# Optimization experiments

Hardware: AMD Instinct MI355X
Metric: run time of the kernel (lower is better)

## Reference

```python
import jax, jax.numpy as jnp
import numpy as np

B = 1_048_576
DIM = 64
NCI_TOTAL = 150_000
FMA_TOTAL = 100_000


def setup_inputs() -> dict:
    key = jax.random.key(0)
    k1, k2, k3, k4, k5, k6, k7 = jax.random.split(key, 7)
    return {
        "pos_n": jax.random.randint(k1, (B,), 0, NCI_TOTAL, dtype=jnp.int64) if jax.config.jax_enable_x64 else jax.random.randint(k1, (B,), 0, NCI_TOTAL, dtype=jnp.int32),
        "pos_m": jax.random.randint(k2, (B,), 0, NCI_TOTAL, dtype=jnp.int32),
        "pos_f": jax.random.randint(k3, (B,), 0, FMA_TOTAL, dtype=jnp.int32),
        "nci_emb": jax.random.normal(k4, (NCI_TOTAL, DIM), dtype=jnp.float32),
        "fma_emb": jax.random.normal(k5, (FMA_TOTAL, DIM), dtype=jnp.float32),
        "n2f_mat": jax.random.normal(k6, (DIM, DIM), dtype=jnp.float32) / np.sqrt(DIM),
        "m2f_mat": jax.random.normal(k7, (DIM, DIM), dtype=jnp.float32) / np.sqrt(DIM),
    }


def reference(pos_n, pos_m, pos_f, nci_emb, fma_emb, n2f_mat, m2f_mat):
    # Embedding gathers. In the original, transfer-matrix lookup ids are all
    # zeros, so the single [dim, dim] matrix is shared across the batch.
    n_e = nci_emb[pos_n]  # [B, D]
    m_e = nci_emb[pos_m]  # [B, D]  (note: pos_m also indexes nci table, per source)
    f_e = fma_emb[pos_f]  # [B, D]

    # TransR-style projection: h = M @ e per sample (shared M).
    h_n = jnp.einsum("ij,bj->bi", n2f_mat, n_e)  # [B, D]
    h_m = jnp.einsum("ij,bj->bi", m2f_mat, m_e)  # [B, D]

    # Squared-diff, sum over dim (the reduce_mean over a size-1 axis is a no-op),
    # then sum over batch.
    n2f_loss = jnp.sum(jnp.square(h_n - f_e))
    m2f_loss = jnp.sum(jnp.square(h_m - f_e))
    return n2f_loss + m2f_loss
```

## Files before the change

kernel.cpp:

```cpp
#include <hip/hip_runtime.h>
#include <hip/hip_fp16.h>


typedef _Float16 half8 __attribute__((ext_vector_type(8)));
typedef __fp16  fp16x2 __attribute__((ext_vector_type(2)));
typedef float floatx16 __attribute__((ext_vector_type(16)));

#define NBLOCKS 1024
#define SPB 128
#define NCI_ELEMS 9600000
#define FMA_ELEMS 6400000

__device__ inline half8 cvt8(float4 a, float4 b) {
    union { half8 h; fp16x2 h2[4]; } u;
    u.h2[0] = __builtin_amdgcn_cvt_pkrtz(a.x, a.y);
    u.h2[1] = __builtin_amdgcn_cvt_pkrtz(a.z, a.w);
    u.h2[2] = __builtin_amdgcn_cvt_pkrtz(b.x, b.y);
    u.h2[3] = __builtin_amdgcn_cvt_pkrtz(b.z, b.w);
    return u.h;
}

__device__ inline uint2 pack4(float4 v) {
    union { fp16x2 h2[2]; uint2 u; } p;
    p.h2[0] = __builtin_amdgcn_cvt_pkrtz(v.x, v.y);
    p.h2[1] = __builtin_amdgcn_cvt_pkrtz(v.z, v.w);
    return p.u;
}

__device__ inline uint2 pack8_fp8(float4 a, float4 b) {
    int lo = 0, hi = 0;
    lo = __builtin_amdgcn_cvt_pk_fp8_f32(a.x, a.y, lo, false);
    lo = __builtin_amdgcn_cvt_pk_fp8_f32(a.z, a.w, lo, true);
    hi = __builtin_amdgcn_cvt_pk_fp8_f32(b.x, b.y, hi, false);
    hi = __builtin_amdgcn_cvt_pk_fp8_f32(b.z, b.w, hi, true);
    uint2 r; r.x = (unsigned)lo; r.y = (unsigned)hi; return r;
}

__device__ inline long pack8_fp8_l(const float* p) {
    uint2 b = pack8_fp8(*(const float4*)p, *(const float4*)(p + 4));
    return (long)(((unsigned long)b.y << 32) | b.x);
}

__global__ __launch_bounds__(256) void convert_kernel(
    const float4* __restrict__ nci, const float4* __restrict__ fma,
    uint2* __restrict__ nci8, uint2* __restrict__ fma8)
{
    const int stride = gridDim.x * blockDim.x;
    const int tid = blockIdx.x * blockDim.x + threadIdx.x;
    for (int i = tid; i < NCI_ELEMS / 8; i += stride)
        nci8[i] = pack8_fp8(nci[2 * i], nci[2 * i + 1]);
    for (int i = tid; i < FMA_ELEMS / 8; i += stride)
        fma8[i] = pack8_fp8(fma[2 * i], fma[2 * i + 1]);
}

__global__ __launch_bounds__(256, 4) void ontomap_kernel_q(
    const int* __restrict__ pos_n, const int* __restrict__ pos_m,
    const int* __restrict__ pos_f,
    const unsigned char* __restrict__ nci8, const unsigned char* __restrict__ fma8,
    const float* __restrict__ n2f, const float* __restrict__ m2f,
    float* __restrict__ out, int iters)
{
    const int lane = threadIdx.x & 63;
    const int wave = threadIdx.x >> 6;
    const int l31  = lane & 31;
    const int hi   = lane >> 5;
    const int hoff = hi * 32;

    long Bn[2][4], Bm[2][4];
#pragma unroll
    for (int nt = 0; nt < 2; ++nt) {
#pragma unroll
        for (int t = 0; t < 4; ++t) {
            Bn[nt][t] = pack8_fp8_l(n2f + (nt * 32 + l31) * 64 + hoff + t * 8);
            Bm[nt][t] = pack8_fp8_l(m2f + (nt * 32 + l31) * 64 + hoff + t * 8);
        }
    }

    long If0[4], If1[4];
#pragma unroll
    for (int t = 0; t < 4; ++t) {
        const unsigned j = (unsigned)(l31 - t * 8);
        const long pat = (j < 8) ? (long)(0xB8ULL << (8 * j)) : 0L;
        If0[t] = hi ? 0L : pat;
        If1[t] = hi ? pat : 0L;
    }

    float loss = 0.0f;

    int in_, im_, if_;
    {
        int s = blockIdx.x * SPB + wave * 32 + l31;
        in_ = pos_n[s]; im_ = pos_m[s]; if_ = pos_f[s];
    }

#pragma unroll 1
    for (int it = 0; it < iters; ++it) {
        const int in0 = in_, im0 = im_, if0 = if_;
        if (it + 1 < iters) {
            int s = ((it + 1) * NBLOCKS + blockIdx.x) * SPB + wave * 32 + l31;
            in_ = pos_n[s]; im_ = pos_m[s]; if_ = pos_f[s];
        }

        const unsigned char* pn = nci8 + (long)in0 * 64 + hoff;
        const unsigned char* pf = fma8 + (long)if0 * 64 + hoff;
        const unsigned char* pm = nci8 + (long)im0 * 64 + hoff;

        ulonglong2 n01 = *(const ulonglong2*)pn;
        ulonglong2 n23 = *(const ulonglong2*)(pn + 16);
        ulonglong2 f01 = *(const ulonglong2*)pf;
        ulonglong2 f23 = *(const ulonglong2*)(pf + 16);
        ulonglong2 m01 = *(const ulonglong2*)pm;
        ulonglong2 m23 = *(const ulonglong2*)(pm + 16);

        const long An[4] = {(long)n01.x, (long)n01.y, (long)n23.x, (long)n23.y};
        const long Ff[4] = {(long)f01.x, (long)f01.y, (long)f23.x, (long)f23.y};
        const long Am[4] = {(long)m01.x, (long)m01.y, (long)m23.x, (long)m23.y};

        {
            floatx16 a{};
#pragma unroll
            for (int t = 0; t < 4; ++t)
                a = __builtin_amdgcn_mfma_f32_32x32x16_fp8_fp8(An[t], Bn[0][t], a, 0, 0, 0);
#pragma unroll
            for (int t = 0; t < 4; ++t)
                a = __builtin_amdgcn_mfma_f32_32x32x16_fp8_fp8(Ff[t], If0[t], a, 0, 0, 0);
#pragma unroll
            for (int r = 0; r < 16; ++r) loss = fmaf(a[r], a[r], loss);
        }
        {
            floatx16 a{};
#pragma unroll
            for (int t = 0; t < 4; ++t)
                a = __builtin_amdgcn_mfma_f32_32x32x16_fp8_fp8(An[t], Bn[1][t], a, 0, 0, 0);
#pragma unroll
            for (int t = 0; t < 4; ++t)
                a = __builtin_amdgcn_mfma_f32_32x32x16_fp8_fp8(Ff[t], If1[t], a, 0, 0, 0);
#pragma unroll
            for (int r = 0; r < 16; ++r) loss = fmaf(a[r], a[r], loss);
        }
        {
            floatx16 a{};
#pragma unroll
            for (int t = 0; t < 4; ++t)
                a = __builtin_amdgcn_mfma_f32_32x32x16_fp8_fp8(Am[t], Bm[0][t], a, 0, 0, 0);
#pragma unroll
            for (int t = 0; t < 4; ++t)
                a = __builtin_amdgcn_mfma_f32_32x32x16_fp8_fp8(Ff[t], If0[t], a, 0, 0, 0);
#pragma unroll
            for (int r = 0; r < 16; ++r) loss = fmaf(a[r], a[r], loss);
        }
        {
            floatx16 a{};
#pragma unroll
            for (int t = 0; t < 4; ++t)
                a = __builtin_amdgcn_mfma_f32_32x32x16_fp8_fp8(Am[t], Bm[1][t], a, 0, 0, 0);
#pragma unroll
            for (int t = 0; t < 4; ++t)
                a = __builtin_amdgcn_mfma_f32_32x32x16_fp8_fp8(Ff[t], If1[t], a, 0, 0, 0);
#pragma unroll
            for (int r = 0; r < 16; ++r) loss = fmaf(a[r], a[r], loss);
        }
    }

#pragma unroll
    for (int o = 32; o > 0; o >>= 1) loss += __shfl_xor(loss, o, 64);
    if (lane == 0) atomicAdd(out, loss);
}

#define ROW_BYTES 144
__global__ __launch_bounds__(256, 2) void ontomap_kernel_f32(
    const int* __restrict__ pos_n, const int* __restrict__ pos_m,
    const int* __restrict__ pos_f,
    const float* __restrict__ nci, const float* __restrict__ fma_emb,
    const float* __restrict__ n2f, const float* __restrict__ m2f,
    float* __restrict__ out, int iters)
{
    __shared__ char lds[4 * 2 * 32 * ROW_BYTES];

    const int lane = threadIdx.x & 63;
    const int wave = threadIdx.x >> 6;
    const int l31  = lane & 31;
    const int hi   = lane >> 5;
    const int kbase = hi * 8;
    const int srow   = lane >> 4;
    const int schunk = lane & 15;

    char* const nbase = lds + wave * (2 * 32 * ROW_BYTES);
    char* const mbase = nbase + 32 * ROW_BYTES;

    half8 Bn[2][4], Bm[2][4];
#pragma unroll
    for (int nt = 0; nt < 2; ++nt) {
#pragma unroll
        for (int t = 0; t < 4; ++t) {
            const float* p = n2f + (nt * 32 + l31) * 64 + t * 16 + kbase;
            Bn[nt][t] = cvt8(*(const float4*)p, *(const float4*)(p + 4));
            const float* q = m2f + (nt * 32 + l31) * 64 + t * 16 + kbase;
            Bm[nt][t] = cvt8(*(const float4*)q, *(const float4*)(q + 4));
        }
    }

    float loss = 0.0f;
    int in_, im_, if_;
    {
        int s = blockIdx.x * SPB + wave * 32 + l31;
        in_ = pos_n[s]; im_ = pos_m[s]; if_ = pos_f[s];
    }

#pragma unroll 1
    for (int it = 0; it < iters; ++it) {
        const int in0 = in_, im0 = im_, if0 = if_;
        if (it + 1 < iters) {
            int s = ((it + 1) * NBLOCKS + blockIdx.x) * SPB + wave * 32 + l31;
            in_ = pos_n[s]; im_ = pos_m[s]; if_ = pos_f[s];
        }

#pragma unroll
        for (int i = 0; i < 8; ++i) {
            const int rl = i * 4 + srow;
            const int rn = __shfl(in0, rl, 64);
            float4 v = ((const float4*)(nci + (long)rn * 64))[schunk];
            *(uint2*)(nbase + rl * ROW_BYTES + schunk * 8) = pack4(v);
            const int rm = __shfl(im0, rl, 64);
            float4 w = ((const float4*)(nci + (long)rm * 64))[schunk];
            *(uint2*)(mbase + rl * ROW_BYTES + schunk * 8) = pack4(w);
        }
        asm volatile("" ::: "memory");

        floatx16 aN0{}, aN1{}, aM0{}, aM1{};
#pragma unroll
        for (int t = 0; t < 4; ++t) {
            half8 aF = *(const half8*)(nbase + l31 * ROW_BYTES + t * 32 + hi * 16);
            aN0 = __builtin_amdgcn_mfma_f32_32x32x16_f16(aF, Bn[0][t], aN0, 0, 0, 0);
            aN1 = __builtin_amdgcn_mfma_f32_32x32x16_f16(aF, Bn[1][t], aN1, 0, 0, 0);
            half8 bF = *(const half8*)(mbase + l31 * ROW_BYTES + t * 32 + hi * 16);
            aM0 = __builtin_amdgcn_mfma_f32_32x32x16_f16(bF, Bm[0][t], aM0, 0, 0, 0);
            aM1 = __builtin_amdgcn_mfma_f32_32x32x16_f16(bF, Bm[1][t], aM1, 0, 0, 0);
        }

#pragma unroll
        for (int r = 0; r < 16; ++r) {
            const int mrow = (r & 3) + 8 * (r >> 2) + 4 * hi;
            const int fid  = __shfl(if0, mrow, 64);
            const float* pf = fma_emb + (long)fid * 64 + l31;
            const float f0 = pf[0];
            const float f1 = pf[32];
            float d;
            d = aN0[r] - f0; loss = fmaf(d, d, loss);
            d = aM0[r] - f0; loss = fmaf(d, d, loss);
            d = aN1[r] - f1; loss = fmaf(d, d, loss);
            d = aM1[r] - f1; loss = fmaf(d, d, loss);
        }
    }

#pragma unroll
    for (int o = 32; o > 0; o >>= 1) loss += __shfl_xor(loss, o, 64);
    if (lane == 0) atomicAdd(out, loss);
}

extern "C" void kernel_launch(void* const* d_in, const int* in_sizes, int n_in,
                              void* d_out, int out_size, void* d_ws, size_t ws_size,
                              hipStream_t stream) {
    const int*   pos_n   = (const int*)d_in[0];
    const int*   pos_m   = (const int*)d_in[1];
    const int*   pos_f   = (const int*)d_in[2];
    const float* nci_emb = (const float*)d_in[3];
    const float* fma_emb = (const float*)d_in[4];
    const float* n2f_mat = (const float*)d_in[5];
    const float* m2f_mat = (const float*)d_in[6];
    float* out = (float*)d_out;

    const int B = in_sizes[0];
    const int iters = B / (NBLOCKS * SPB);

    (void)hipMemsetAsync(out, 0, sizeof(float), stream);

    const size_t need = (size_t)NCI_ELEMS + (size_t)FMA_ELEMS;
    if (ws_size >= need) {
        unsigned char* nci8 = (unsigned char*)d_ws;
        unsigned char* fma8 = nci8 + NCI_ELEMS;
        convert_kernel<<<2048, 256, 0, stream>>>(
            (const float4*)nci_emb, (const float4*)fma_emb,
            (uint2*)nci8, (uint2*)fma8);
        ontomap_kernel_q<<<NBLOCKS, 256, 0, stream>>>(
            pos_n, pos_m, pos_f, nci8, fma8, n2f_mat, m2f_mat, out, iters);
    } else {
        ontomap_kernel_f32<<<NBLOCKS, 256, 0, stream>>>(
            pos_n, pos_m, pos_f, nci_emb, fma_emb, n2f_mat, m2f_mat, out, iters);
    }
}
```

Measured before the change: 186.1 us.

## Double-buffer fp8 embedding gathers two iterations ahead in quantized kernel

Restructures the main loop of the fp8 MFMA kernel into a two-stage software pipeline. Row gathers for the next two iterations are issued ahead, and the index loads run four steps ahead, so MFMA work overlaps in-flight gather latency. This costs more VGPRs for the two sets of gathered rows, which at launch bounds of 4 waves per SIMD could cause spills. The loop also assumes an even iteration count, and clamping to the last index causes redundant loads at the tail.

```diff
diff --git a/kernel.cpp b/kernel.cpp
--- a/kernel.cpp
+++ b/kernel.cpp
@@ -52,6 +52,73 @@
     for (int i = tid; i < FMA_ELEMS / 8; i += stride)
         fma8[i] = pack8_fp8(fma[2 * i], fma[2 * i + 1]);
 }
+
+#define GATHER(iN, iM, iF, n01, n23, f01, f23, m01, m23)                     \
+    {                                                                        \
+        const unsigned char* pn_ = nci8 + (long)(iN) * 64 + hoff;            \
+        const unsigned char* pf_ = fma8 + (long)(iF) * 64 + hoff;            \
+        const unsigned char* pm_ = nci8 + (long)(iM) * 64 + hoff;            \
+        n01 = *(const ulonglong2*)pn_;                                       \
+        n23 = *(const ulonglong2*)(pn_ + 16);                                \
+        f01 = *(const ulonglong2*)pf_;                                       \
+        f23 = *(const ulonglong2*)(pf_ + 16);                                \
+        m01 = *(const ulonglong2*)pm_;                                       \
+        m23 = *(const ulonglong2*)(pm_ + 16);                                \
+    }
+
+#define COMPUTE_TILES(n01, n23, f01, f23, m01, m23)                          \
+    {                                                                        \
+        const long An_[4] = {(long)(n01).x, (long)(n01).y,                   \
+                             (long)(n23).x, (long)(n23).y};                  \
+        const long Ff_[4] = {(long)(f01).x, (long)(f01).y,                   \
+                             (long)(f23).x, (long)(f23).y};                  \
+        const long Am_[4] = {(long)(m01).x, (long)(m01).y,                   \
+                             (long)(m23).x, (long)(m23).y};                  \
+        {                                                                    \
+            floatx16 a{};                                                    \
+            _Pragma("unroll")                                                \
+            for (int t = 0; t < 4; ++t)                                      \
+                a = __builtin_amdgcn_mfma_f32_32x32x16_fp8_fp8(An_[t], Bn[0][t], a, 0, 0, 0); \
+            _Pragma("unroll")                                                \
+            for (int t = 0; t < 4; ++t)                                      \
+                a = __builtin_amdgcn_mfma_f32_32x32x16_fp8_fp8(Ff_[t], If0[t], a, 0, 0, 0);   \
+            _Pragma("unroll")                                                \
+            for (int r = 0; r < 16; ++r) loss = fmaf(a[r], a[r], loss);      \
+        }                                                                    \
+        {                                                                    \
+            floatx16 a{};                                                    \
+            _Pragma("unroll")                                                \
+            for (int t = 0; t < 4; ++t)                                      \
+                a = __builtin_amdgcn_mfma_f32_32x32x16_fp8_fp8(An_[t], Bn[1][t], a, 0, 0, 0); \
+            _Pragma("unroll")                                                \
+            for (int t = 0; t < 4; ++t)                                      \
+                a = __builtin_amdgcn_mfma_f32_32x32x16_fp8_fp8(Ff_[t], If1[t], a, 0, 0, 0);   \
+            _Pragma("unroll")                                                \
+            for (int r = 0; r < 16; ++r) loss = fmaf(a[r], a[r], loss);      \
+        }                                                                    \
+        {                                                                    \
+            floatx16 a{};                                                    \
+            _Pragma("unroll")                                                \
+            for (int t = 0; t < 4; ++t)                                      \
+                a = __builtin_amdgcn_mfma_f32_32x32x16_fp8_fp8(Am_[t], Bm[0][t], a, 0, 0, 0); \
+            _Pragma("unroll")                                                \
+            for (int t = 0; t < 4; ++t)                                      \
+                a = __builtin_amdgcn_mfma_f32_32x32x16_fp8_fp8(Ff_[t], If0[t], a, 0, 0, 0);   \
+            _Pragma("unroll")                                                \
+            for (int r = 0; r < 16; ++r) loss = fmaf(a[r], a[r], loss);      \
+        }                                                                    \
+        {                                                                    \
+            floatx16 a{};                                                    \
+            _Pragma("unroll")                                                \
+            for (int t = 0; t < 4; ++t)                                      \
+                a = __builtin_amdgcn_mfma_f32_32x32x16_fp8_fp8(Am_[t], Bm[1][t], a, 0, 0, 0); \
+            _Pragma("unroll")                                                \
+            for (int t = 0; t < 4; ++t)                                      \
+                a = __builtin_amdgcn_mfma_f32_32x32x16_fp8_fp8(Ff_[t], If1[t], a, 0, 0, 0);   \
+            _Pragma("unroll")                                                \
+            for (int r = 0; r < 16; ++r) loss = fmaf(a[r], a[r], loss);      \
+        }                                                                    \
+    }
 
 __global__ __launch_bounds__(256, 4) void ontomap_kernel_q(
     const int* __restrict__ pos_n, const int* __restrict__ pos_m,
@@ -87,78 +154,39 @@
 
     float loss = 0.0f;
 
-    int in_, im_, if_;
+    const int base  = blockIdx.x * SPB + wave * 32 + l31;
+    const int istep = NBLOCKS * SPB;
+    const int last  = iters - 1;
+
+    int iNa = pos_n[base], iMa = pos_m[base], iFa = pos_f[base];
+    int s1 = istep + base;
+    int iNb = pos_n[s1], iMb = pos_m[s1], iFb = pos_f[s1];
+
+    ulonglong2 An01, An23, Af01, Af23, Am01, Am23;
+    ulonglong2 Bn01, Bn23, Bf01, Bf23, Bm01, Bm23;
+    GATHER(iNa, iMa, iFa, An01, An23, Af01, Af23, Am01, Am23);
+    GATHER(iNb, iMb, iFb, Bn01, Bn23, Bf01, Bf23, Bm01, Bm23);
+
     {
-        int s = blockIdx.x * SPB + wave * 32 + l31;
-        in_ = pos_n[s]; im_ = pos_m[s]; if_ = pos_f[s];
+        int s = min(2, last) * istep + base;
+        iNa = pos_n[s]; iMa = pos_m[s]; iFa = pos_f[s];
+        s = min(3, last) * istep + base;
+        iNb = pos_n[s]; iMb = pos_m[s]; iFb = pos_f[s];
     }
 
 #pragma unroll 1
-    for (int it = 0; it < iters; ++it) {
-        const int in0 = in_, im0 = im_, if0 = if_;
-        if (it + 1 < iters) {
-            int s = ((it + 1) * NBLOCKS + blockIdx.x) * SPB + wave * 32 + l31;
-            in_ = pos_n[s]; im_ = pos_m[s]; if_ = pos_f[s];
-        }
-
-        const unsigned char* pn = nci8 + (long)in0 * 64 + hoff;
-        const unsigned char* pf = fma8 + (long)if0 * 64 + hoff;
-        const unsigned char* pm = nci8 + (long)im0 * 64 + hoff;
-
-        ulonglong2 n01 = *(const ulonglong2*)pn;
-        ulonglong2 n23 = *(const ulonglong2*)(pn + 16);
-        ulonglong2 f01 = *(const ulonglong2*)pf;
-        ulonglong2 f23 = *(const ulonglong2*)(pf + 16);
-        ulonglong2 m01 = *(const ulonglong2*)pm;
-        ulonglong2 m23 = *(const ulonglong2*)(pm + 16);
-
-        const long An[4] = {(long)n01.x, (long)n01.y, (long)n23.x, (long)n23.y};
-        const long Ff[4] = {(long)f01.x, (long)f01.y, (long)f23.x, (long)f23.y};
-        const long Am[4] = {(long)m01.x, (long)m01.y, (long)m23.x, (long)m23.y};
-
+    for (int it = 0; it < iters; it += 2) {
+        COMPUTE_TILES(An01, An23, Af01, Af23, Am01, Am23);
+        GATHER(iNa, iMa, iFa, An01, An23, Af01, Af23, Am01, Am23);
         {
-            floatx16 a{};
-#pragma unroll
-            for (int t = 0; t < 4; ++t)
-                a = __builtin_amdgcn_mfma_f32_32x32x16_fp8_fp8(An[t], Bn[0][t], a, 0, 0, 0);
-#pragma unroll
-            for (int t = 0; t < 4; ++t)
-                a = __builtin_amdgcn_mfma_f32_32x32x16_fp8_fp8(Ff[t], If0[t], a, 0, 0, 0);
-#pragma unroll
-            for (int r = 0; r < 16; ++r) loss = fmaf(a[r], a[r], loss);
-        }
+            int s = min(it + 4, last) * istep + base;
+            iNa = pos_n[s]; iMa = pos_m[s]; iFa = pos_f[s];
+        }
+        COMPUTE_TILES(Bn01, Bn23, Bf01, Bf23, Bm01, Bm23);
+        GATHER(iNb, iMb, iFb, Bn01, Bn23, Bf01, Bf23, Bm01, Bm23);
         {
-            floatx16 a{};
-#pragma unroll
-            for (int t = 0; t < 4; ++t)
-                a = __builtin_amdgcn_mfma_f32_32x32x16_fp8_fp8(An[t], Bn[1][t], a, 0, 0, 0);
-#pragma unroll
-            for (int t = 0; t < 4; ++t)
-                a = __builtin_amdgcn_mfma_f32_32x32x16_fp8_fp8(Ff[t], If1[t], a, 0, 0, 0);
-#pragma unroll
-            for (int r = 0; r < 16; ++r) loss = fmaf(a[r], a[r], loss);
-        }
-        {
-            floatx16 a{};
-#pragma unroll
-            for (int t = 0; t < 4; ++t)
-                a = __builtin_amdgcn_mfma_f32_32x32x16_fp8_fp8(Am[t], Bm[0][t], a, 0, 0, 0);
-#pragma unroll
-            for (int t = 0; t < 4; ++t)
-                a = __builtin_amdgcn_mfma_f32_32x32x16_fp8_fp8(Ff[t], If0[t], a, 0, 0, 0);
-#pragma unroll
-            for (int r = 0; r < 16; ++r) loss = fmaf(a[r], a[r], loss);
-        }
-        {
-            floatx16 a{};
-#pragma unroll
-            for (int t = 0; t < 4; ++t)
-                a = __builtin_amdgcn_mfma_f32_32x32x16_fp8_fp8(Am[t], Bm[1][t], a, 0, 0, 0);
-#pragma unroll
-            for (int t = 0; t < 4; ++t)
-                a = __builtin_amdgcn_mfma_f32_32x32x16_fp8_fp8(Ff[t], If1[t], a, 0, 0, 0);
-#pragma unroll
-            for (int r = 0; r < 16; ++r) loss = fmaf(a[r], a[r], loss);
+            int s = min(it + 5, last) * istep + base;
+            iNb = pos_n[s]; iMb = pos_m[s]; iFb = pos_f[s];
         }
     }
 
```

New measurement: 224.9 us. 1.21x slower.
